# Performance work log

Measured on AMD Instinct MI355X. Metric: run time of the kernel, lower is better.

## Reference

```python
import jax, jax.numpy as jnp
import numpy as np

B, S, D, H = 2, 2048, 1024, 16
DK = D // H


def setup_inputs() -> dict:
    key = jax.random.key(0)
    ks = jax.random.split(key, 12)
    scale = 0.02
    inp = {
        "query": jax.random.normal(ks[0], (B, S, D), jnp.float32),
        "key": jax.random.normal(ks[1], (B, S, D), jnp.float32),
        "value": jax.random.normal(ks[2], (B, S, D), jnp.float32),
        "mask": jax.random.randint(ks[3], (B, S), 0, 2, jnp.int32),
        "Wq": jax.random.normal(ks[4], (D, D), jnp.float32) * scale,
        "bq": jnp.zeros((D,), jnp.float32),
        "Wk": jax.random.normal(ks[5], (D, D), jnp.float32) * scale,
        "bk": jnp.zeros((D,), jnp.float32),
        "Wv": jax.random.normal(ks[6], (D, D), jnp.float32) * scale,
        "bv": jnp.zeros((D,), jnp.float32),
        "Wo": jax.random.normal(ks[7], (D, D), jnp.float32) * scale,
        "bo": jnp.zeros((D,), jnp.float32),
    }
    return inp


def reference(query, key, value, mask, Wq, bq, Wk, bk, Wv, bv, Wo, bo):
    # Linear projections then split heads: [B, S, D] -> [B, H, S, DK]
    def proj(x, W, b):
        y = x @ W.T + b  # torch nn.Linear: x @ W^T + b
        return y.reshape(B, S, H, DK).transpose(0, 2, 1, 3)

    q = proj(query, Wq, bq)
    k = proj(key, Wk, bk)
    v = proj(value, Wv, bv)

    # Scaled dot-product attention with full [B, H, S, S] scores (naive form)
    scores = jnp.einsum("bhqd,bhkd->bhqk", q, k) / jnp.sqrt(jnp.float32(DK))
    # mask==1 marks padding over key positions; broadcast [B,1,1,S]
    pad = (mask == 1)[:, None, None, :]
    scores = jnp.where(pad, -jnp.inf, scores)
    p_attn = jax.nn.softmax(scores, axis=-1)
    # dropout omitted (eval / deterministic mode)
    x = jnp.einsum("bhqk,bhkd->bhqd", p_attn, v)
    x = x.transpose(0, 2, 1, 3).reshape(B, S, D)
    return x @ Wo.T + bo
```

## Files before the change

kernel.cpp:

```cpp
#include <hip/hip_runtime.h>
#include <stdint.h>
#include <type_traits>

typedef short bf16x8 __attribute__((ext_vector_type(8)));
typedef float f32x4  __attribute__((ext_vector_type(4)));
typedef unsigned int u32x2 __attribute__((ext_vector_type(2)));
typedef unsigned short u16;

#define BB 2
#define SS 2048
#define DD 1024
#define HH 16
#define NTOK (BB*SS)
#define QSC 0.18033688f

__device__ __forceinline__ u16 f2bf(float f) {
  union { float f; uint32_t u; } c; c.f = f;
  uint32_t r = c.u + 0x7FFFu + ((c.u >> 16) & 1u);
  return (u16)(r >> 16);
}

__device__ __forceinline__ void gll16(const void* g, void* l) {
  __builtin_amdgcn_global_load_lds((__attribute__((address_space(1))) void*)(void*)g,
                                   (__attribute__((address_space(3))) void*)l, 16, 0, 0);
}

struct CvtArgs { const float* src[4]; u16* dst[4]; int n; };
__global__ void cvtn_kernel(CvtArgs a) {
  const float* __restrict__ src = a.src[blockIdx.z];
  u16* __restrict__ dst = a.dst[blockIdx.z];
  int i = (blockIdx.x * blockDim.x + threadIdx.x) * 4;
  const int stride = gridDim.x * blockDim.x * 4;
  for (; i < a.n; i += stride) {
    float4 v = *(const float4*)(src + i);
    ushort4 o;
    o.x = f2bf(v.x); o.y = f2bf(v.y); o.z = f2bf(v.z); o.w = f2bf(v.w);
    *(ushort4*)(dst + i) = o;
  }
}

__global__ __launch_bounds__(256) void maskcnt_kernel(const int* __restrict__ mask,
                                                      float* __restrict__ out) {
  const int b = blockIdx.x, t = threadIdx.x;
  const int4 v1 = *(const int4*)(mask + b * SS + t * 8);
  const int4 v2 = *(const int4*)(mask + b * SS + t * 8 + 4);
  int s = v1.x + v1.y + v1.z + v1.w + v2.x + v2.y + v2.z + v2.w;
#pragma unroll
  for (int off = 32; off; off >>= 1) s += __shfl_xor(s, off);
  __shared__ int red[4];
  if ((t & 63) == 0) red[t >> 6] = s;
  __syncthreads();
  if (t == 0) out[b] = (float)(red[0] + red[1] + red[2] + red[3]);
}

template<int MODE>
__device__ __forceinline__ void gemm_bt_body(const u16* __restrict__ A,
                                             const u16* __restrict__ W,
                                             const float* __restrict__ bias,
                                             const int* __restrict__ mask,
                                             void* __restrict__ Cout,
                                             int m0, int n0,
                                             u16* As, u16* Bs) {
  const int tid = threadIdx.x;
  const int lane = tid & 63, wid = tid >> 6;
  const int r16 = lane & 15, g4 = lane >> 4;
  const int wm = (wid >> 1) * 64, wn = (wid & 1) * 64;

  const f32x4 zero = {0.f, 0.f, 0.f, 0.f};
  f32x4 acc[4][4];
#pragma unroll
  for (int i = 0; i < 4; ++i)
#pragma unroll
    for (int j = 0; j < 4; ++j) acc[i][j] = zero;

  const int row0 = tid >> 2, blk0 = tid & 3;
  auto stage = [&](int kt, int buf) {
#pragma unroll
    for (int it = 0; it < 2; ++it) {
      const int row = row0 + it * 64;
      const int sb = blk0 ^ (row & 3);
      gll16(A + (size_t)(m0 + row) * DD + kt * 32 + sb * 8,
            As + buf * 4096 + (tid + it * 256) * 8);
      gll16(W + (size_t)(n0 + row) * DD + kt * 32 + sb * 8,
            Bs + buf * 4096 + (tid + it * 256) * 8);
    }
  };

  stage(0, 0);
  __syncthreads();

  for (int kt = 0; kt < DD / 32; ++kt) {
    const int cur = kt & 1;
    if (kt + 1 < DD / 32) stage(kt + 1, cur ^ 1);

    bf16x8 af[4], bfr[4];
#pragma unroll
    for (int i = 0; i < 4; ++i) {
      const int ar = wm + i * 16 + r16;
      af[i] = *(const bf16x8*)(As + cur * 4096 + ar * 32 + ((g4 ^ (ar & 3)) << 3));
      const int br = wn + i * 16 + r16;
      bfr[i] = *(const bf16x8*)(Bs + cur * 4096 + br * 32 + ((g4 ^ (br & 3)) << 3));
    }
#pragma unroll
    for (int i = 0; i < 4; ++i)
#pragma unroll
      for (int j = 0; j < 4; ++j)
        acc[i][j] = __builtin_amdgcn_mfma_f32_16x16x32_bf16(af[i], bfr[j], acc[i][j], 0, 0, 0);
    __syncthreads();
  }

  float bcol[4];
#pragma unroll
  for (int j = 0; j < 4; ++j) bcol[j] = bias[n0 + wn + j * 16 + r16];

#pragma unroll
  for (int i = 0; i < 4; ++i) {
    const int rowb = m0 + wm + i * 16 + g4 * 4;
    int mr[4] = {0, 0, 0, 0};
    if (MODE == 1 || MODE == 2) {
      const int4 mv = *(const int4*)(mask + rowb);
      mr[0] = mv.x; mr[1] = mv.y; mr[2] = mv.z; mr[3] = mv.w;
    }
#pragma unroll
    for (int j = 0; j < 4; ++j) {
      const int col = n0 + wn + j * 16 + r16;
      if (MODE == 3) {
#pragma unroll
        for (int r = 0; r < 4; ++r)
          ((float*)Cout)[(size_t)(rowb + r) * DD + col] = acc[i][j][r] + bcol[j];
      } else if (MODE == 0) {
#pragma unroll
        for (int r = 0; r < 4; ++r)
          ((u16*)Cout)[(size_t)(rowb + r) * DD + col] = f2bf((acc[i][j][r] + bcol[j]) * QSC);
      } else if (MODE == 1) {
#pragma unroll
        for (int r = 0; r < 4; ++r) {
          const float v = mr[r] ? 0.f : (acc[i][j][r] + bcol[j]);
          ((u16*)Cout)[(size_t)(rowb + r) * DD + col] = f2bf(v);
        }
      } else {
        const int bb = rowb >> 11, s0 = rowb & (SS - 1);
        ushort4 pk;
        pk.x = f2bf(mr[0] ? 0.f : (acc[i][j][0] + bcol[j]));
        pk.y = f2bf(mr[1] ? 0.f : (acc[i][j][1] + bcol[j]));
        pk.z = f2bf(mr[2] ? 0.f : (acc[i][j][2] + bcol[j]));
        pk.w = f2bf(mr[3] ? 0.f : (acc[i][j][3] + bcol[j]));
        *(ushort4*)((u16*)Cout + (size_t)(bb * DD + col) * SS + s0) = pk;
      }
    }
  }
}

struct QkvArgs {
  const u16* A[3];
  const u16* W[3];
  const float* bias[3];
  const int* mask;
  u16* outq; u16* outk; u16* outv;
};

__global__ __launch_bounds__(256) void gemm_qkv_kernel(QkvArgs a) {
  __shared__ __align__(16) u16 As[2][128 * 32];
  __shared__ __align__(16) u16 Bs[2][128 * 32];
  const int fid = blockIdx.x + (blockIdx.y << 3) + (blockIdx.z << 8);
  const int swz = (fid & 7) * 96 + (fid >> 3);
  const int z = swz >> 8;
  const int rem = swz & 255;
  const int m0 = (rem >> 3) * 128, n0 = (rem & 7) * 128;
  if (z == 0)      gemm_bt_body<0>(a.A[0], a.W[0], a.bias[0], nullptr, (void*)a.outq, m0, n0, &As[0][0], &Bs[0][0]);
  else if (z == 1) gemm_bt_body<1>(a.A[1], a.W[1], a.bias[1], a.mask, (void*)a.outk, m0, n0, &As[0][0], &Bs[0][0]);
  else             gemm_bt_body<2>(a.A[2], a.W[2], a.bias[2], a.mask, (void*)a.outv, m0, n0, &As[0][0], &Bs[0][0]);
}

__global__ __launch_bounds__(256) void gemm_out_kernel(const u16* __restrict__ A,
                                                       const u16* __restrict__ W,
                                                       const float* __restrict__ bias,
                                                       float* __restrict__ C) {
  __shared__ __align__(16) u16 As[2][128 * 32];
  __shared__ __align__(16) u16 Bs[2][128 * 32];
  const int fid = blockIdx.x + (blockIdx.y << 3);
  const int swz = (fid & 7) * 32 + (fid >> 3);
  const int m0 = (swz >> 3) * 128, n0 = (swz & 7) * 128;
  gemm_bt_body<3>(A, W, bias, nullptr, (void*)C, m0, n0, &As[0][0], &Bs[0][0]);
}

#define NT (SS / 64)
__global__ __launch_bounds__(256) void attn_kernel(const u16* __restrict__ Qp,
                                                   const u16* __restrict__ Kp,
                                                   const u16* __restrict__ Vt,
                                                   const float* __restrict__ padcnt,
                                                   u16* __restrict__ ctx) {
  __shared__ __align__(16) u16 Ks[2][64 * 64];
  __shared__ __align__(16) u16 Vs[2][64 * 64];

  const int tid = threadIdx.x;
  const int lane = tid & 63, wid = tid >> 6;
  const int r16 = lane & 15, g4 = lane >> 4;
  const int fid = blockIdx.x + 32 * (blockIdx.y + 16 * blockIdx.z);
  const int swz = (fid & 7) * 128 + (fid >> 3);
  const int qt = swz & 31, rem = swz >> 5;
  const int h = rem & 15, b = rem >> 4;

  const int qtok = b * SS + qt * 64 + wid * 16 + r16;
  bf16x8 qf[2];
#pragma unroll
  for (int c = 0; c < 2; ++c)
    qf[c] = *(const bf16x8*)(Qp + (size_t)qtok * DD + h * 64 + c * 32 + g4 * 8);

  const f32x4 zero = {0.f, 0.f, 0.f, 0.f};
  f32x4 o[4];
#pragma unroll
  for (int j = 0; j < 4; ++j) o[j] = zero;
  float ll = 0.f;

  const int srow0 = tid >> 3, sblk0 = tid & 7;
  const u16* Kbase = Kp + (size_t)(b * SS) * DD + h * 64;
  const u16* Vbase = Vt + (size_t)(b * DD + h * 64) * SS;

  auto stage = [&](int kt, int buf) {
#pragma unroll
    for (int it = 0; it < 2; ++it) {
      const int row = srow0 + it * 32;
      const int sb = sblk0 ^ (row & 7);
      gll16(Kbase + (size_t)(kt * 64 + row) * DD + sb * 8, &Ks[buf][(tid + it * 256) * 8]);
      gll16(Vbase + (size_t)row * SS + kt * 64 + sb * 8, &Vs[buf][(tid + it * 256) * 8]);
    }
  };

  stage(0, 0);
  __syncthreads();

  auto tile_step = [&](auto CURC, int kt) {
    constexpr int cur = decltype(CURC)::value;
    if (kt + 1 < NT) stage(kt + 1, cur ^ 1);

    f32x4 st[4];
    __builtin_amdgcn_s_setprio(1);
#pragma unroll
    for (int j = 0; j < 4; ++j) {
      const int kr = j * 16 + r16;
      const bf16x8 kf = *(const bf16x8*)(&Ks[cur][kr * 64 + ((g4 ^ (kr & 7)) << 3)]);
      st[j] = __builtin_amdgcn_mfma_f32_16x16x32_bf16(kf, qf[0], zero, 0, 0, 0);
    }
#pragma unroll
    for (int j = 0; j < 4; ++j) {
      const int kr = j * 16 + r16;
      const bf16x8 kf = *(const bf16x8*)(&Ks[cur][kr * 64 + (((4 + g4) ^ (kr & 7)) << 3)]);
      st[j] = __builtin_amdgcn_mfma_f32_16x16x32_bf16(kf, qf[1], st[j], 0, 0, 0);
    }
    __builtin_amdgcn_s_setprio(0);

    uint32_t q0[4], q1[4];
#pragma unroll
    for (int j = 0; j < 4; ++j) {
      float p0, p1, p2, p3;
      asm("v_exp_f32 %0, %1" : "=v"(p0) : "v"(st[j][0]));
      asm("v_exp_f32 %0, %1" : "=v"(p1) : "v"(st[j][1]));
      asm("v_exp_f32 %0, %1" : "=v"(p2) : "v"(st[j][2]));
      asm("v_exp_f32 %0, %1" : "=v"(p3) : "v"(st[j][3]));
      ll += (p0 + p1) + (p2 + p3);
      asm("v_cvt_pk_bf16_f32 %0, %1, %2" : "=v"(q0[j]) : "v"(p0), "v"(p1));
      asm("v_cvt_pk_bf16_f32 %0, %1, %2" : "=v"(q1[j]) : "v"(p2), "v"(p3));
    }

    bf16x8 pa[2];
#pragma unroll
    for (int c = 0; c < 2; ++c) {
      u32x2 s0 = __builtin_amdgcn_permlane32_swap(q0[2 * c], q0[2 * c + 1], false, false);
      u32x2 s1 = __builtin_amdgcn_permlane16_swap(s0.x, s0.y, false, false);
      u32x2 t0 = __builtin_amdgcn_permlane32_swap(q1[2 * c], q1[2 * c + 1], false, false);
      u32x2 t1 = __builtin_amdgcn_permlane16_swap(t0.x, t0.y, false, false);
      union { uint32_t u[4]; bf16x8 v; } cv;
      cv.u[0] = s1.x; cv.u[1] = t1.x; cv.u[2] = s1.y; cv.u[3] = t1.y;
      pa[c] = cv.v;
    }

    __builtin_amdgcn_s_setprio(1);
#pragma unroll
    for (int c = 0; c < 2; ++c)
#pragma unroll
      for (int j = 0; j < 4; ++j) {
        const int vr = j * 16 + r16;
        const bf16x8 vf = *(const bf16x8*)(&Vs[cur][vr * 64 + (((c * 4 + g4) ^ (vr & 7)) << 3)]);
        o[j] = __builtin_amdgcn_mfma_f32_16x16x32_bf16(pa[c], vf, o[j], 0, 0, 0);
      }
    __builtin_amdgcn_s_setprio(0);
    __syncthreads();
  };

  for (int kt = 0; kt < NT; kt += 2) {
    tile_step(std::integral_constant<int, 0>{}, kt);
    tile_step(std::integral_constant<int, 1>{}, kt + 1);
  }

  ll += __shfl_xor(ll, 16);
  ll += __shfl_xor(ll, 32);
  ll -= padcnt[b];
  const float inv = 1.0f / ll;
  float invr[4];
#pragma unroll
  for (int r = 0; r < 4; ++r) invr[r] = __shfl(inv, g4 * 4 + r);

  const int otok = b * SS + qt * 64 + wid * 16 + g4 * 4;
#pragma unroll
  for (int j = 0; j < 4; ++j) {
    const int col = h * 64 + j * 16 + r16;
#pragma unroll
    for (int r = 0; r < 4; ++r)
      ctx[(size_t)(otok + r) * DD + col] = f2bf(o[j][r] * invr[r]);
  }
}

extern "C" void kernel_launch(void* const* d_in, const int* in_sizes, int n_in,
                              void* d_out, int out_size, void* d_ws, size_t ws_size,
                              hipStream_t stream) {
  (void)in_sizes; (void)n_in; (void)out_size; (void)ws_size;
  const float* f_q = (const float*)d_in[0];
  const float* f_k = (const float*)d_in[1];
  const float* f_v = (const float*)d_in[2];
  const int* mask  = (const int*)d_in[3];
  const float* Wq = (const float*)d_in[4];
  const float* bq = (const float*)d_in[5];
  const float* Wk = (const float*)d_in[6];
  const float* bk = (const float*)d_in[7];
  const float* Wv = (const float*)d_in[8];
  const float* bv = (const float*)d_in[9];
  const float* Wo = (const float*)d_in[10];
  const float* bo = (const float*)d_in[11];

  char* ws = (char*)d_ws;
  const size_t XB = (size_t)NTOK * DD * 2;
  const size_t WB = (size_t)DD * DD * 2;
  u16* Xq  = (u16*)(ws);
  u16* Xk  = (u16*)(ws + XB);
  u16* Xv  = (u16*)(ws + 2 * XB);
  u16* Qp  = (u16*)(ws + 3 * XB);
  u16* Kp  = (u16*)(ws + 4 * XB);
  u16* Vt  = (u16*)(ws + 5 * XB);
  u16* Wqb = (u16*)(ws + 6 * XB);
  u16* Wkb = (u16*)(ws + 6 * XB + WB);
  u16* Wvb = (u16*)(ws + 6 * XB + 2 * WB);
  u16* Wob = (u16*)(ws + 6 * XB + 3 * WB);
  float* padcnt = (float*)(ws + 6 * XB + 4 * WB);
  u16* ctx = Xq;

  CvtArgs cx;
  cx.src[0] = f_q; cx.src[1] = f_k; cx.src[2] = f_v; cx.src[3] = f_q;
  cx.dst[0] = Xq;  cx.dst[1] = Xk;  cx.dst[2] = Xv;  cx.dst[3] = Xq;
  cx.n = NTOK * DD;
  cvtn_kernel<<<dim3(1024, 1, 3), 256, 0, stream>>>(cx);

  CvtArgs cw;
  cw.src[0] = Wq;  cw.src[1] = Wk;  cw.src[2] = Wv;  cw.src[3] = Wo;
  cw.dst[0] = Wqb; cw.dst[1] = Wkb; cw.dst[2] = Wvb; cw.dst[3] = Wob;
  cw.n = DD * DD;
  cvtn_kernel<<<dim3(256, 1, 4), 256, 0, stream>>>(cw);

  maskcnt_kernel<<<BB, 256, 0, stream>>>(mask, padcnt);

  QkvArgs qa;
  qa.A[0] = Xq;  qa.A[1] = Xk;  qa.A[2] = Xv;
  qa.W[0] = Wqb; qa.W[1] = Wkb; qa.W[2] = Wvb;
  qa.bias[0] = bq; qa.bias[1] = bk; qa.bias[2] = bv;
  qa.mask = mask;
  qa.outq = Qp; qa.outk = Kp; qa.outv = Vt;
  gemm_qkv_kernel<<<dim3(DD / 128, NTOK / 128, 3), 256, 0, stream>>>(qa);

  attn_kernel<<<dim3(SS / 64, HH, BB), 256, 0, stream>>>(Qp, Kp, Vt, padcnt, ctx);
  gemm_out_kernel<<<dim3(DD / 128, NTOK / 128), 256, 0, stream>>>(ctx, Wob, bo, (float*)d_out);
}
```

Before: 142.4 us.

## Fuse fp32-to-bf16 activation conversion into QKV GEMM loads

The separate conversion kernel for query/key/value activations is removed. The QKV GEMM now streams fp32 tiles into LDS via global_load_lds and converts them to bf16 with v_cvt_pk_bf16_f32 when reading MFMA fragments. This avoids writing and rereading three bf16 activation buffers, at the cost of doubled LDS footprint and global read bytes for A inside the GEMM. Staging loops also switch to incrementing pointers with unrolled double-buffer steps in the GEMM and attention kernels to cut address arithmetic.

```diff
diff --git a/kernel.cpp b/kernel.cpp
--- a/kernel.cpp
+++ b/kernel.cpp
@@ -54,13 +54,13 @@
 }
 
 template<int MODE>
-__device__ __forceinline__ void gemm_bt_body(const u16* __restrict__ A,
-                                             const u16* __restrict__ W,
-                                             const float* __restrict__ bias,
-                                             const int* __restrict__ mask,
-                                             void* __restrict__ Cout,
-                                             int m0, int n0,
-                                             u16* As, u16* Bs) {
+__device__ __forceinline__ void gemm_qkv_body(const float* __restrict__ A,
+                                              const u16* __restrict__ W,
+                                              const float* __restrict__ bias,
+                                              const int* __restrict__ mask,
+                                              u16* __restrict__ Cout,
+                                              int m0, int n0,
+                                              float* Af, u16* Bs) {
   const int tid = threadIdx.x;
   const int lane = tid & 63, wid = tid >> 6;
   const int r16 = lane & 15, g4 = lane >> 4;
@@ -73,31 +73,57 @@
 #pragma unroll
     for (int j = 0; j < 4; ++j) acc[i][j] = zero;
 
-  const int row0 = tid >> 2, blk0 = tid & 3;
-  auto stage = [&](int kt, int buf) {
-#pragma unroll
-    for (int it = 0; it < 2; ++it) {
-      const int row = row0 + it * 64;
-      const int sb = blk0 ^ (row & 3);
-      gll16(A + (size_t)(m0 + row) * DD + kt * 32 + sb * 8,
-            As + buf * 4096 + (tid + it * 256) * 8);
-      gll16(W + (size_t)(n0 + row) * DD + kt * 32 + sb * 8,
-            Bs + buf * 4096 + (tid + it * 256) * 8);
-    }
-  };
-
-  stage(0, 0);
+  const float* aptr[4];
+  {
+    const int rowa = tid >> 3, blka = tid & 7;
+#pragma unroll
+    for (int it = 0; it < 4; ++it) {
+      const int row = rowa + it * 32;
+      aptr[it] = A + (size_t)(m0 + row) * DD + ((blka ^ (row & 7)) << 2);
+    }
+  }
+  const u16* wptr[2];
+  {
+    const int roww = tid >> 2, blkw = tid & 3;
+#pragma unroll
+    for (int it = 0; it < 2; ++it) {
+      const int row = roww + it * 64;
+      wptr[it] = W + (size_t)(n0 + row) * DD + ((blkw ^ (row & 3)) << 3);
+    }
+  }
+  auto stage = [&](int buf) {
+#pragma unroll
+    for (int it = 0; it < 4; ++it) {
+      gll16(aptr[it], Af + buf * 4096 + (tid + it * 256) * 4);
+      aptr[it] += 32;
+    }
+#pragma unroll
+    for (int it = 0; it < 2; ++it) {
+      gll16(wptr[it], Bs + buf * 4096 + (tid + it * 256) * 8);
+      wptr[it] += 32;
+    }
+  };
+
+  stage(0);
   __syncthreads();
 
-  for (int kt = 0; kt < DD / 32; ++kt) {
-    const int cur = kt & 1;
-    if (kt + 1 < DD / 32) stage(kt + 1, cur ^ 1);
-
+  auto kstep = [&](auto CURC, int kt) {
+    constexpr int cur = decltype(CURC)::value;
+    if (kt + 1 < 32) stage(cur ^ 1);
     bf16x8 af[4], bfr[4];
 #pragma unroll
     for (int i = 0; i < 4; ++i) {
       const int ar = wm + i * 16 + r16;
-      af[i] = *(const bf16x8*)(As + cur * 4096 + ar * 32 + ((g4 ^ (ar & 3)) << 3));
+      const int x = ar & 7;
+      const float* arow = Af + cur * 4096 + ar * 32;
+      const f32x4 lo = *(const f32x4*)(arow + (((g4 * 2) ^ x) << 2));
+      const f32x4 hi = *(const f32x4*)(arow + (((g4 * 2 + 1) ^ x) << 2));
+      union { uint32_t u[4]; bf16x8 v; } cv;
+      asm("v_cvt_pk_bf16_f32 %0, %1, %2" : "=v"(cv.u[0]) : "v"(lo[0]), "v"(lo[1]));
+      asm("v_cvt_pk_bf16_f32 %0, %1, %2" : "=v"(cv.u[1]) : "v"(lo[2]), "v"(lo[3]));
+      asm("v_cvt_pk_bf16_f32 %0, %1, %2" : "=v"(cv.u[2]) : "v"(hi[0]), "v"(hi[1]));
+      asm("v_cvt_pk_bf16_f32 %0, %1, %2" : "=v"(cv.u[3]) : "v"(hi[2]), "v"(hi[3]));
+      af[i] = cv.v;
       const int br = wn + i * 16 + r16;
       bfr[i] = *(const bf16x8*)(Bs + cur * 4096 + br * 32 + ((g4 ^ (br & 3)) << 3));
     }
@@ -107,6 +133,10 @@
       for (int j = 0; j < 4; ++j)
         acc[i][j] = __builtin_amdgcn_mfma_f32_16x16x32_bf16(af[i], bfr[j], acc[i][j], 0, 0, 0);
     __syncthreads();
+  };
+  for (int kt = 0; kt < 32; kt += 2) {
+    kstep(std::integral_constant<int, 0>{}, kt);
+    kstep(std::integral_constant<int, 1>{}, kt + 1);
   }
 
   float bcol[4];
@@ -124,19 +154,15 @@
 #pragma unroll
     for (int j = 0; j < 4; ++j) {
       const int col = n0 + wn + j * 16 + r16;
-      if (MODE == 3) {
+      if (MODE == 0) {
 #pragma unroll
         for (int r = 0; r < 4; ++r)
-          ((float*)Cout)[(size_t)(rowb + r) * DD + col] = acc[i][j][r] + bcol[j];
-      } else if (MODE == 0) {
-#pragma unroll
-        for (int r = 0; r < 4; ++r)
-          ((u16*)Cout)[(size_t)(rowb + r) * DD + col] = f2bf((acc[i][j][r] + bcol[j]) * QSC);
+          Cout[(size_t)(rowb + r) * DD + col] = f2bf((acc[i][j][r] + bcol[j]) * QSC);
       } else if (MODE == 1) {
 #pragma unroll
         for (int r = 0; r < 4; ++r) {
           const float v = mr[r] ? 0.f : (acc[i][j][r] + bcol[j]);
-          ((u16*)Cout)[(size_t)(rowb + r) * DD + col] = f2bf(v);
+          Cout[(size_t)(rowb + r) * DD + col] = f2bf(v);
         }
       } else {
         const int bb = rowb >> 11, s0 = rowb & (SS - 1);
@@ -145,14 +171,14 @@
         pk.y = f2bf(mr[1] ? 0.f : (acc[i][j][1] + bcol[j]));
         pk.z = f2bf(mr[2] ? 0.f : (acc[i][j][2] + bcol[j]));
         pk.w = f2bf(mr[3] ? 0.f : (acc[i][j][3] + bcol[j]));
-        *(ushort4*)((u16*)Cout + (size_t)(bb * DD + col) * SS + s0) = pk;
+        *(ushort4*)(Cout + (size_t)(bb * DD + col) * SS + s0) = pk;
       }
     }
   }
 }
 
 struct QkvArgs {
-  const u16* A[3];
+  const float* A[3];
   const u16* W[3];
   const float* bias[3];
   const int* mask;
@@ -160,28 +186,101 @@
 };
 
 __global__ __launch_bounds__(256) void gemm_qkv_kernel(QkvArgs a) {
-  __shared__ __align__(16) u16 As[2][128 * 32];
-  __shared__ __align__(16) u16 Bs[2][128 * 32];
+  __shared__ __align__(16) float Af[2][4096];
+  __shared__ __align__(16) u16 Bs[2][4096];
   const int fid = blockIdx.x + (blockIdx.y << 3) + (blockIdx.z << 8);
   const int swz = (fid & 7) * 96 + (fid >> 3);
   const int z = swz >> 8;
   const int rem = swz & 255;
   const int m0 = (rem >> 3) * 128, n0 = (rem & 7) * 128;
-  if (z == 0)      gemm_bt_body<0>(a.A[0], a.W[0], a.bias[0], nullptr, (void*)a.outq, m0, n0, &As[0][0], &Bs[0][0]);
-  else if (z == 1) gemm_bt_body<1>(a.A[1], a.W[1], a.bias[1], a.mask, (void*)a.outk, m0, n0, &As[0][0], &Bs[0][0]);
-  else             gemm_bt_body<2>(a.A[2], a.W[2], a.bias[2], a.mask, (void*)a.outv, m0, n0, &As[0][0], &Bs[0][0]);
+  if (z == 0)      gemm_qkv_body<0>(a.A[0], a.W[0], a.bias[0], nullptr, a.outq, m0, n0, &Af[0][0], &Bs[0][0]);
+  else if (z == 1) gemm_qkv_body<1>(a.A[1], a.W[1], a.bias[1], a.mask, a.outk, m0, n0, &Af[0][0], &Bs[0][0]);
+  else             gemm_qkv_body<2>(a.A[2], a.W[2], a.bias[2], a.mask, a.outv, m0, n0, &Af[0][0], &Bs[0][0]);
 }
 
 __global__ __launch_bounds__(256) void gemm_out_kernel(const u16* __restrict__ A,
                                                        const u16* __restrict__ W,
                                                        const float* __restrict__ bias,
                                                        float* __restrict__ C) {
-  __shared__ __align__(16) u16 As[2][128 * 32];
-  __shared__ __align__(16) u16 Bs[2][128 * 32];
+  __shared__ __align__(16) u16 As[2][4096];
+  __shared__ __align__(16) u16 Bs[2][4096];
   const int fid = blockIdx.x + (blockIdx.y << 3);
   const int swz = (fid & 7) * 32 + (fid >> 3);
   const int m0 = (swz >> 3) * 128, n0 = (swz & 7) * 128;
-  gemm_bt_body<3>(A, W, bias, nullptr, (void*)C, m0, n0, &As[0][0], &Bs[0][0]);
+
+  const int tid = threadIdx.x;
+  const int lane = tid & 63, wid = tid >> 6;
+  const int r16 = lane & 15, g4 = lane >> 4;
+  const int wm = (wid >> 1) * 64, wn = (wid & 1) * 64;
+
+  const f32x4 zero = {0.f, 0.f, 0.f, 0.f};
+  f32x4 acc[4][4];
+#pragma unroll
+  for (int i = 0; i < 4; ++i)
+#pragma unroll
+    for (int j = 0; j < 4; ++j) acc[i][j] = zero;
+
+  const u16* aptr[2];
+  const u16* wptr[2];
+  {
+    const int row0 = tid >> 2, blk0 = tid & 3;
+#pragma unroll
+    for (int it = 0; it < 2; ++it) {
+      const int row = row0 + it * 64;
+      const int sb = blk0 ^ (row & 3);
+      aptr[it] = A + (size_t)(m0 + row) * DD + sb * 8;
+      wptr[it] = W + (size_t)(n0 + row) * DD + sb * 8;
+    }
+  }
+  auto stage = [&](int buf) {
+#pragma unroll
+    for (int it = 0; it < 2; ++it) {
+      gll16(aptr[it], &As[buf][(tid + it * 256) * 8]);
+      gll16(wptr[it], &Bs[buf][(tid + it * 256) * 8]);
+      aptr[it] += 32; wptr[it] += 32;
+    }
+  };
+
+  stage(0);
+  __syncthreads();
+
+  auto kstep = [&](auto CURC, int kt) {
+    constexpr int cur = decltype(CURC)::value;
+    if (kt + 1 < 32) stage(cur ^ 1);
+    bf16x8 af[4], bfr[4];
+#pragma unroll
+    for (int i = 0; i < 4; ++i) {
+      const int ar = wm + i * 16 + r16;
+      af[i] = *(const bf16x8*)(&As[cur][ar * 32 + ((g4 ^ (ar & 3)) << 3)]);
+      const int br = wn + i * 16 + r16;
+      bfr[i] = *(const bf16x8*)(&Bs[cur][br * 32 + ((g4 ^ (br & 3)) << 3)]);
+    }
+#pragma unroll
+    for (int i = 0; i < 4; ++i)
+#pragma unroll
+      for (int j = 0; j < 4; ++j)
+        acc[i][j] = __builtin_amdgcn_mfma_f32_16x16x32_bf16(af[i], bfr[j], acc[i][j], 0, 0, 0);
+    __syncthreads();
+  };
+  for (int kt = 0; kt < 32; kt += 2) {
+    kstep(std::integral_constant<int, 0>{}, kt);
+    kstep(std::integral_constant<int, 1>{}, kt + 1);
+  }
+
+  float bcol[4];
+#pragma unroll
+  for (int j = 0; j < 4; ++j) bcol[j] = bias[n0 + wn + j * 16 + r16];
+#pragma unroll
+  for (int i = 0; i < 4; ++i) {
+    const int rowb = m0 + wm + i * 16 + g4 * 4;
+#pragma unroll
+    for (int j = 0; j < 4; ++j) {
+      const int col = n0 + wn + j * 16 + r16;
+#pragma unroll
+      for (int r = 0; r < 4; ++r)
+        C[(size_t)(rowb + r) * DD + col] = acc[i][j][r] + bcol[j];
+    }
+  }
 }
 
 #define NT (SS / 64)
@@ -213,26 +312,34 @@
   for (int j = 0; j < 4; ++j) o[j] = zero;
   float ll = 0.f;
 
-  const int srow0 = tid >> 3, sblk0 = tid & 7;
-  const u16* Kbase = Kp + (size_t)(b * SS) * DD + h * 64;
-  const u16* Vbase = Vt + (size_t)(b * DD + h * 64) * SS;
-
-  auto stage = [&](int kt, int buf) {
+  const u16* kptr[2];
+  const u16* vptr[2];
+  {
+    const int srow0 = tid >> 3, sblk0 = tid & 7;
 #pragma unroll
     for (int it = 0; it < 2; ++it) {
       const int row = srow0 + it * 32;
       const int sb = sblk0 ^ (row & 7);
-      gll16(Kbase + (size_t)(kt * 64 + row) * DD + sb * 8, &Ks[buf][(tid + it * 256) * 8]);
-      gll16(Vbase + (size_t)row * SS + kt * 64 + sb * 8, &Vs[buf][(tid + it * 256) * 8]);
-    }
-  };
-
-  stage(0, 0);
+      kptr[it] = Kp + (size_t)(b * SS + row) * DD + h * 64 + sb * 8;
+      vptr[it] = Vt + (size_t)(b * DD + h * 64 + row) * SS + sb * 8;
+    }
+  }
+  auto stage = [&](int buf) {
+#pragma unroll
+    for (int it = 0; it < 2; ++it) {
+      gll16(kptr[it], &Ks[buf][(tid + it * 256) * 8]);
+      gll16(vptr[it], &Vs[buf][(tid + it * 256) * 8]);
+      kptr[it] += 64 * DD;
+      vptr[it] += 64;
+    }
+  };
+
+  stage(0);
   __syncthreads();
 
   auto tile_step = [&](auto CURC, int kt) {
     constexpr int cur = decltype(CURC)::value;
-    if (kt + 1 < NT) stage(kt + 1, cur ^ 1);
+    if (kt + 1 < NT) stage(cur ^ 1);
 
     f32x4 st[4];
     __builtin_amdgcn_s_setprio(1);
@@ -331,24 +438,15 @@
   char* ws = (char*)d_ws;
   const size_t XB = (size_t)NTOK * DD * 2;
   const size_t WB = (size_t)DD * DD * 2;
-  u16* Xq  = (u16*)(ws);
-  u16* Xk  = (u16*)(ws + XB);
-  u16* Xv  = (u16*)(ws + 2 * XB);
-  u16* Qp  = (u16*)(ws + 3 * XB);
-  u16* Kp  = (u16*)(ws + 4 * XB);
-  u16* Vt  = (u16*)(ws + 5 * XB);
-  u16* Wqb = (u16*)(ws + 6 * XB);
-  u16* Wkb = (u16*)(ws + 6 * XB + WB);
-  u16* Wvb = (u16*)(ws + 6 * XB + 2 * WB);
-  u16* Wob = (u16*)(ws + 6 * XB + 3 * WB);
-  float* padcnt = (float*)(ws + 6 * XB + 4 * WB);
-  u16* ctx = Xq;
-
-  CvtArgs cx;
-  cx.src[0] = f_q; cx.src[1] = f_k; cx.src[2] = f_v; cx.src[3] = f_q;
-  cx.dst[0] = Xq;  cx.dst[1] = Xk;  cx.dst[2] = Xv;  cx.dst[3] = Xq;
-  cx.n = NTOK * DD;
-  cvtn_kernel<<<dim3(1024, 1, 3), 256, 0, stream>>>(cx);
+  u16* ctx = (u16*)(ws);
+  u16* Qp  = (u16*)(ws + XB);
+  u16* Kp  = (u16*)(ws + 2 * XB);
+  u16* Vt  = (u16*)(ws + 3 * XB);
+  u16* Wqb = (u16*)(ws + 4 * XB);
+  u16* Wkb = (u16*)(ws + 4 * XB + WB);
+  u16* Wvb = (u16*)(ws + 4 * XB + 2 * WB);
+  u16* Wob = (u16*)(ws + 4 * XB + 3 * WB);
+  float* padcnt = (float*)(ws + 4 * XB + 4 * WB);
 
   CvtArgs cw;
   cw.src[0] = Wq;  cw.src[1] = Wk;  cw.src[2] = Wv;  cw.src[3] = Wo;
@@ -359,7 +457,7 @@
   maskcnt_kernel<<<BB, 256, 0, stream>>>(mask, padcnt);
 
   QkvArgs qa;
-  qa.A[0] = Xq;  qa.A[1] = Xk;  qa.A[2] = Xv;
+  qa.A[0] = f_q; qa.A[1] = f_k; qa.A[2] = f_v;
   qa.W[0] = Wqb; qa.W[1] = Wkb; qa.W[2] = Wvb;
   qa.bias[0] = bq; qa.bias[1] = bk; qa.bias[2] = bv;
   qa.mask = mask;
```

Result: slower. 146.2 us (+2.7%).
